# Optimization experiments

Measured on AMD Instinct MI355X. Metric: run time of the kernel, lower is better.

Reference implementation:

```python
import jax, jax.numpy as jnp
import numpy as np

N_NODES = 100000
N_EDGES = 1600000
IN_FEATS = 128
NUM_HEADS = 4
OUT_FEATS = 32
NUM_ETYPES = 8
DROP_BLOCKS = 4


def setup_inputs() -> dict:
    key = jax.random.key(0)
    k1, k2, k3, k4, k5 = jax.random.split(key, 5)
    feat = jax.random.normal(k1, (N_NODES, IN_FEATS), dtype=jnp.float32)
    e_feat = jax.random.randint(k2, (N_EDGES,), 0, NUM_ETYPES, dtype=jnp.int32)
    src = jax.random.randint(k3, (N_EDGES,), 0, N_NODES, dtype=jnp.int32)
    dst = jax.random.randint(k4, (N_EDGES,), 0, N_NODES, dtype=jnp.int32)
    kf, ke = jax.random.split(k5)
    # xavier_normal with relu gain for fc: std = gain * sqrt(2/(fan_in+fan_out))
    gain = float(np.sqrt(2.0))
    std = gain * float(np.sqrt(2.0 / (IN_FEATS + NUM_HEADS * OUT_FEATS)))
    fc_weight = jax.random.normal(kf, (NUM_HEADS * OUT_FEATS, IN_FEATS), dtype=jnp.float32) * std
    # edge_emb initialized with normal_()
    edge_emb = jax.random.normal(ke, (NUM_ETYPES, NUM_HEADS), dtype=jnp.float32)
    return {"feat": feat, "fc_weight": fc_weight, "edge_emb": edge_emb,
            "e_feat": e_feat, "src": src, "dst": dst, "drop_blocks": DROP_BLOCKS}


def _edge_softmax(e, dst, n_nodes):
    # segmented softmax over incoming edges per destination node, per head
    # e: (E, H)
    m = jax.ops.segment_max(e, dst, num_segments=n_nodes)      # (N, H)
    z = jnp.exp(e - m[dst])                                    # (E, H)
    s = jax.ops.segment_sum(z, dst, num_segments=n_nodes)      # (N, H)
    return z / s[dst]


def reference(feat, fc_weight, edge_emb, e_feat, src, dst, drop_blocks):
    n = feat.shape[0]
    H = edge_emb.shape[1]
    D = fc_weight.shape[0] // H
    # fc projection -> (N, H, D); feat_drop is identity (p=0 / eval)
    ft = (feat @ fc_weight.T).reshape(n, H, D)
    # edge type embedding logits (E, H)
    ee = edge_emb[e_feat]
    attn = _edge_softmax(ee, dst, n)                           # (E, H)
    # mcdropedge with attn_drop p=0: attn broadcast over blocks is identity scaling
    # u_mul_e + sum: gather src features, scale by attn, scatter-sum into dst
    msg = ft[src] * attn[:, :, None]                           # (E, H, D)
    rst = jax.ops.segment_sum(msg, dst, num_segments=n)        # (N, H, D)
    # attn returned with mcdropedge expansion shape (E, H, drop_blocks, 1)
    attn_out = jnp.broadcast_to(attn[:, :, None], (attn.shape[0], H, drop_blocks))[..., None]
    return rst, attn_out
```

## Files before the change

kernel.cpp:

```cpp
#include <hip/hip_runtime.h>


typedef short short8 __attribute__((ext_vector_type(8)));
typedef unsigned short ushort8 __attribute__((ext_vector_type(8)));
typedef float f32x4 __attribute__((ext_vector_type(4)));

__device__ inline unsigned short f2bf(float x) {
    unsigned u = __builtin_bit_cast(unsigned, x);
    u += 0x7FFFu + ((u >> 16) & 1u);
    return (unsigned short)(u >> 16);
}

__device__ inline void nt_store4(float* p, float a, float b, float c, float d) {
    f32x4 v = (f32x4){a, b, c, d};
    __builtin_nontemporal_store(v, (f32x4*)p);
}

__global__ __launch_bounds__(256) void k_bcnt(const int* __restrict__ dst,
                                              unsigned* __restrict__ gpart, int E) {
    __shared__ unsigned l[256];
    int tid = threadIdx.x;
    l[tid] = 0;
    __syncthreads();
    int base = blockIdx.x * 4096;
#pragma unroll
    for (int j = 0; j < 16; ++j) {
        int e = base + j * 256 + tid;
        if (e < E) atomicAdd(&l[(unsigned)dst[e] >> 9], 1u);
    }
    __syncthreads();
    gpart[blockIdx.x * 256 + tid] = l[tid];
}

__global__ __launch_bounds__(256) void k_bscan(const unsigned* __restrict__ gpart,
                                               int nchunk,
                                               unsigned* __restrict__ gbase,
                                               unsigned* __restrict__ gcur) {
    __shared__ unsigned s[256];
    int t = threadIdx.x;
    unsigned sum = 0;
    int r = 0;
    for (; r + 4 <= nchunk; r += 4) {
        unsigned a0 = gpart[(r + 0) * 256 + t];
        unsigned a1 = gpart[(r + 1) * 256 + t];
        unsigned a2 = gpart[(r + 2) * 256 + t];
        unsigned a3 = gpart[(r + 3) * 256 + t];
        sum += a0 + a1 + a2 + a3;
    }
    for (; r < nchunk; ++r) sum += gpart[r * 256 + t];
    unsigned orig = sum;
    s[t] = sum;
    __syncthreads();
    for (int of = 1; of < 256; of <<= 1) {
        unsigned v = (t >= of) ? s[t - of] : 0u;
        __syncthreads();
        s[t] += v;
        __syncthreads();
    }
    unsigned eb = s[t] - orig;
    gbase[t] = eb;
    gcur[t] = eb;
}

__global__ __launch_bounds__(256) void k_part(const int* __restrict__ src,
                                              const int* __restrict__ dst,
                                              const int* __restrict__ ef,
                                              unsigned* __restrict__ gcur,
                                              unsigned* __restrict__ csr2,
                                              int E, int nbuk) {
    __shared__ unsigned lcnt[256];
    __shared__ unsigned lbase[256];
    __shared__ unsigned lcur[256];
    __shared__ unsigned gw2[256];
    __shared__ unsigned stp[4096];
    __shared__ unsigned short stb[4096];
    int tid = threadIdx.x;
    lcnt[tid] = 0;
    __syncthreads();

    int cb = blockIdx.x * 4096;
    int cc = E - cb; if (cc > 4096) cc = 4096;

    unsigned pay[16];
    unsigned short bk[16];
#pragma unroll
    for (int j = 0; j < 16; ++j) {
        int idx = j * 256 + tid;
        if (idx < cc) {
            int e = cb + idx;
            unsigned d = (unsigned)dst[e];
            pay[j] = (unsigned)src[e] | ((unsigned)ef[e] << 17) | ((d & 511u) << 20);
            bk[j] = (unsigned short)(d >> 9);
            atomicAdd(&lcnt[bk[j]], 1u);
        }
    }
    __syncthreads();
    lbase[tid] = lcnt[tid];
    __syncthreads();
    for (int of = 1; of < 256; of <<= 1) {
        unsigned v = (tid >= of) ? lbase[tid - of] : 0u;
        __syncthreads();
        lbase[tid] += v;
        __syncthreads();
    }
    unsigned eb = lbase[tid] - lcnt[tid];
    __syncthreads();
    lbase[tid] = eb;
    lcur[tid] = eb;
    __syncthreads();
#pragma unroll
    for (int j = 0; j < 16; ++j) {
        int idx = j * 256 + tid;
        if (idx < cc) {
            unsigned lpos = atomicAdd(&lcur[bk[j]], 1u);
            stp[lpos] = pay[j];
            stb[lpos] = bk[j];
        }
    }
    if (tid < nbuk && lcnt[tid]) gw2[tid] = atomicAdd(&gcur[tid], lcnt[tid]);
    __syncthreads();
#pragma unroll
    for (int j = 0; j < 16; ++j) {
        int i = j * 256 + tid;
        if (i < cc) {
            unsigned b = stb[i];
            csr2[gw2[b] + (i - lbase[b])] = stp[i];
        }
    }
}

__global__ __launch_bounds__(256) void k_bsort2(const unsigned* __restrict__ csr2,
                                                const unsigned* __restrict__ gbase,
                                                const unsigned* __restrict__ gend,
                                                const float* __restrict__ emb,
                                                unsigned* __restrict__ csr,
                                                unsigned* __restrict__ offs,
                                                unsigned* __restrict__ deg,
                                                float* __restrict__ stats, int N) {
    __shared__ unsigned cnt8[512 * 8];
    __shared__ unsigned degL[512];
    __shared__ unsigned offsL[512];
    __shared__ unsigned curL[512];
    __shared__ unsigned tmp[256];
    __shared__ float se[32];
    int b = blockIdx.x, tid = threadIdx.x;
    if (tid < 32) se[tid] = emb[tid];
#pragma unroll
    for (int i = 0; i < 16; ++i) cnt8[i * 256 + tid] = 0u;
    __syncthreads();
    unsigned r0 = gbase[b], r1 = gend[b];
    for (unsigned i = r0 + tid; i < r1; i += 256) {
        unsigned en = csr2[i];
        atomicAdd(&cnt8[((en >> 20) & 511u) * 8u + ((en >> 17) & 7u)], 1u);
    }
    __syncthreads();
    int n0 = tid * 2, n1 = tid * 2 + 1;
    unsigned d0 = 0, d1 = 0;
#pragma unroll
    for (int k = 0; k < 8; ++k) { d0 += cnt8[n0 * 8 + k]; d1 += cnt8[n1 * 8 + k]; }
    degL[n0] = d0; degL[n1] = d1;
    tmp[tid] = d0 + d1;
    __syncthreads();
    for (int of = 1; of < 256; of <<= 1) {
        unsigned v = (tid >= of) ? tmp[tid - of] : 0u;
        __syncthreads();
        tmp[tid] += v;
        __syncthreads();
    }
    unsigned eb = tmp[tid] - (d0 + d1);
    offsL[n0] = eb;        curL[n0] = eb;
    offsL[n1] = eb + d0;   curL[n1] = eb + d0;
#pragma unroll
    for (int q = 0; q < 2; ++q) {
        int nl = tid * 2 + q;
        int gn = b * 512 + nl;
        if (gn < N) {
            offs[gn] = r0 + offsL[nl];
            unsigned dg = degL[nl];
            deg[gn] = dg;
            const unsigned* c = &cnt8[nl * 8];
#pragma unroll
            for (int h = 0; h < 4; ++h) {
                float m = -3.4e38f;
#pragma unroll
                for (int tt = 0; tt < 8; ++tt)
                    if (c[tt]) m = fmaxf(m, se[tt * 4 + h]);
                float s = 0.f;
#pragma unroll
                for (int tt = 0; tt < 8; ++tt)
                    if (c[tt]) s += (float)c[tt] * expf(se[tt * 4 + h] - m);
                stats[(size_t)gn * 8 + h] = m;
                stats[(size_t)gn * 8 + 4 + h] = dg ? (1.0f / s) : 0.0f;
            }
        }
    }
    __syncthreads();
    for (unsigned i = r0 + tid; i < r1; i += 256) {
        unsigned en = csr2[i];
        unsigned nlo = (en >> 20) & 511u;
        unsigned tt = (en >> 17) & 7u;
        unsigned pos = r0 + atomicAdd(&curL[nlo], 1u);
        csr[pos] = (en & 0x1FFFFu) | (tt << 20);
    }
}

__global__ __launch_bounds__(256) void k_attn_out(const int* __restrict__ e_feat,
                                                  const int* __restrict__ dst,
                                                  const float* __restrict__ emb,
                                                  const float* __restrict__ stats,
                                                  float* __restrict__ ao, int E) {
    __shared__ float av[4 * 257];
    int tid = threadIdx.x;
    int e = blockIdx.x * 256 + tid;
    float a0 = 0.f, a1 = 0.f, a2 = 0.f, a3 = 0.f;
    if (e < E) {
        int tt = e_feat[e];
        int d = dst[e];
        const float4* st4 = (const float4*)(stats + (size_t)d * 8);
        float4 m4 = st4[0], i4 = st4[1];
        float4 ee = *(const float4*)(emb + tt * 4);
        a0 = expf(ee.x - m4.x) * i4.x;
        a1 = expf(ee.y - m4.y) * i4.y;
        a2 = expf(ee.z - m4.z) * i4.z;
        a3 = expf(ee.w - m4.w) * i4.w;
    }
    av[0 * 257 + tid] = a0;
    av[1 * 257 + tid] = a1;
    av[2 * 257 + tid] = a2;
    av[3 * 257 + tid] = a3;
    __syncthreads();
    size_t base = (size_t)blockIdx.x * 1024;
    size_t lim = (size_t)E * 4;
#pragma unroll
    for (int r = 0; r < 4; ++r) {
        size_t g = base + r * 256 + tid;
        if (g < lim) {
            int gl = r * 256 + tid;
            float v = av[(gl & 3) * 257 + (gl >> 2)];
            nt_store4(ao + g * 4, v, v, v, v);
        }
    }
}

__global__ __launch_bounds__(256) void k_gemm_mfma(const float* __restrict__ feat,
                                                   const float* __restrict__ W,
                                                   unsigned short* __restrict__ ftb, int N) {
    __shared__ unsigned short Sb[128 * 136];
    int tid = threadIdx.x;
    int row0 = blockIdx.x * 128;

#pragma unroll
    for (int it = 0; it < 16; ++it) {
        int i = it * 1024 + tid * 4;
        int r = i >> 7, c = i & 127;
        unsigned swz = (unsigned)((r & 7) << 4);
        float4 w4 = *(const float4*)(W + i);
        ushort4 wb;
        wb.x = f2bf(w4.x); wb.y = f2bf(w4.y); wb.z = f2bf(w4.z); wb.w = f2bf(w4.w);
        *(ushort4*)((char*)Sb + (((unsigned)(r * 256 + c * 2)) ^ swz)) = wb;
    }
    __syncthreads();

    int wv = tid >> 6, lane = tid & 63;
    int rl = lane & 15;
    unsigned swz = (unsigned)((lane & 7) << 4);
    int kq = (lane >> 4) * 16;
    int ko = (lane >> 4) * 8;

    int ra0 = row0 + wv * 32 + rl;
    int ra1 = ra0 + 16;
    bool v0 = ra0 < N, v1 = ra1 < N;
    const float* ap0 = feat + (size_t)ra0 * 128 + ko;
    const float* ap1 = feat + (size_t)ra1 * 128 + ko;

    f32x4 acc[2][8];
#pragma unroll
    for (int rt = 0; rt < 2; ++rt)
#pragma unroll
        for (int jt = 0; jt < 8; ++jt)
            acc[rt][jt] = (f32x4){0.f, 0.f, 0.f, 0.f};

    const char* Bb = (const char*)Sb;
#pragma unroll
    for (int kk = 0; kk < 4; ++kk) {
        int kb = kk * 64 + kq;
        short8 a[2], bfr[8];
#pragma unroll
        for (int rt = 0; rt < 2; ++rt) {
            const float* ap = rt ? ap1 : ap0;
            bool v = rt ? v1 : v0;
            float4 lo = make_float4(0.f, 0.f, 0.f, 0.f), hi = lo;
            if (v) { lo = *(const float4*)(ap + kk * 32); hi = *(const float4*)(ap + kk * 32 + 4); }
            short8 t;
            t[0] = (short)f2bf(lo.x); t[1] = (short)f2bf(lo.y);
            t[2] = (short)f2bf(lo.z); t[3] = (short)f2bf(lo.w);
            t[4] = (short)f2bf(hi.x); t[5] = (short)f2bf(hi.y);
            t[6] = (short)f2bf(hi.z); t[7] = (short)f2bf(hi.w);
            a[rt] = t;
        }
#pragma unroll
        for (int jt = 0; jt < 8; ++jt)
            bfr[jt] = *(const short8*)(Bb + (((unsigned)((jt * 16 + rl) * 256 + kb)) ^ swz));
#pragma unroll
        for (int rt = 0; rt < 2; ++rt)
#pragma unroll
            for (int jt = 0; jt < 8; ++jt)
                acc[rt][jt] = __builtin_amdgcn_mfma_f32_16x16x32_bf16(a[rt], bfr[jt], acc[rt][jt], 0, 0, 0);
    }

    __syncthreads();
#pragma unroll
    for (int rt = 0; rt < 2; ++rt) {
        int rbase = wv * 32 + rt * 16 + ((lane >> 4) << 2);
#pragma unroll
        for (int jt = 0; jt < 8; ++jt) {
            int col = jt * 16 + rl;
#pragma unroll
            for (int rg = 0; rg < 4; ++rg)
                Sb[(rbase + rg) * 136 + col] = f2bf(acc[rt][jt][rg]);
        }
    }
    __syncthreads();
#pragma unroll
    for (int g = 0; g < 8; ++g) {
        int rloc = g * 16 + (tid >> 4);
        int cc = (tid & 15) * 8;
        int gr = row0 + rloc;
        if (gr < N) {
            ushort8 v = *(const ushort8*)(&Sb[rloc * 136 + cc]);
            *(ushort8*)(ftb + (size_t)gr * 128 + cc) = v;
        }
    }
}

__global__ __launch_bounds__(256) void k_agg(const unsigned* __restrict__ csr,
                                             const unsigned* __restrict__ offs,
                                             const unsigned* __restrict__ deg,
                                             const float* __restrict__ stats,
                                             const float* __restrict__ emb,
                                             const uint4* __restrict__ ft4,
                                             float* __restrict__ rst, int N) {
    __shared__ float wl[4 * 32];
    int tid = threadIdx.x;
    int wv = tid >> 6, lane = tid & 63;
    int n = blockIdx.x * 4 + wv;
    n = __builtin_amdgcn_readfirstlane(n);
    if (n < N && lane < 32) {
        int tt = lane >> 2, hh = lane & 3;
        float m = stats[(size_t)n * 8 + hh];
        float is = stats[(size_t)n * 8 + 4 + hh];
        wl[wv * 32 + lane] = expf(emb[tt * 4 + hh] - m) * is;
    }
    __syncthreads();
    if (n >= N) return;
    unsigned o = offs[n], dg = deg[n];
    int cl = lane & 15;
    int es = lane >> 4;
    int h = cl >> 2;
    const float* wlh = wl + wv * 32 + h;
    float acc[8];
#pragma unroll
    for (int i = 0; i < 8; ++i) acc[i] = 0.f;

    for (unsigned kb = 0; kb < dg; kb += 64) {
        unsigned rem = dg - kb; if (rem > 64) rem = 64;
        unsigned centry = 0;
        if (lane < (int)rem) centry = csr[o + kb + lane];
        unsigned g = 0;
        for (; g + 16 <= rem; g += 16) {
            uint4 f[4]; float a[4];
#pragma unroll
            for (int q = 0; q < 4; ++q) {
                unsigned e = __shfl(centry, (int)(g + q * 4 + es), 64);
                f[q] = ft4[(size_t)(e & 0xFFFFFu) * 16 + cl];
                a[q] = wlh[(e >> 20) * 4];
            }
#pragma unroll
            for (int q = 0; q < 4; ++q) {
                acc[0] = fmaf(a[q], __builtin_bit_cast(float, f[q].x << 16), acc[0]);
                acc[1] = fmaf(a[q], __builtin_bit_cast(float, f[q].x & 0xFFFF0000u), acc[1]);
                acc[2] = fmaf(a[q], __builtin_bit_cast(float, f[q].y << 16), acc[2]);
                acc[3] = fmaf(a[q], __builtin_bit_cast(float, f[q].y & 0xFFFF0000u), acc[3]);
                acc[4] = fmaf(a[q], __builtin_bit_cast(float, f[q].z << 16), acc[4]);
                acc[5] = fmaf(a[q], __builtin_bit_cast(float, f[q].z & 0xFFFF0000u), acc[5]);
                acc[6] = fmaf(a[q], __builtin_bit_cast(float, f[q].w << 16), acc[6]);
                acc[7] = fmaf(a[q], __builtin_bit_cast(float, f[q].w & 0xFFFF0000u), acc[7]);
            }
        }
        for (; g < rem; g += 4) {
            int eidx = (int)g + es;
            bool valid = eidx < (int)rem;
            unsigned e = __shfl(centry, valid ? eidx : (int)g, 64);
            uint4 f = ft4[(size_t)(e & 0xFFFFFu) * 16 + cl];
            float a = valid ? wlh[(e >> 20) * 4] : 0.f;
            acc[0] = fmaf(a, __builtin_bit_cast(float, f.x << 16), acc[0]);
            acc[1] = fmaf(a, __builtin_bit_cast(float, f.x & 0xFFFF0000u), acc[1]);
            acc[2] = fmaf(a, __builtin_bit_cast(float, f.y << 16), acc[2]);
            acc[3] = fmaf(a, __builtin_bit_cast(float, f.y & 0xFFFF0000u), acc[3]);
            acc[4] = fmaf(a, __builtin_bit_cast(float, f.z << 16), acc[4]);
            acc[5] = fmaf(a, __builtin_bit_cast(float, f.z & 0xFFFF0000u), acc[5]);
            acc[6] = fmaf(a, __builtin_bit_cast(float, f.w << 16), acc[6]);
            acc[7] = fmaf(a, __builtin_bit_cast(float, f.w & 0xFFFF0000u), acc[7]);
        }
    }
#pragma unroll
    for (int i = 0; i < 8; ++i) {
        acc[i] += __shfl_xor(acc[i], 16, 64);
        acc[i] += __shfl_xor(acc[i], 32, 64);
    }
    if (lane < 16) {
        float* op = rst + (size_t)n * 128 + cl * 8;
        nt_store4(op, acc[0], acc[1], acc[2], acc[3]);
        nt_store4(op + 4, acc[4], acc[5], acc[6], acc[7]);
    }
}

extern "C" void kernel_launch(void* const* d_in, const int* in_sizes, int n_in,
                              void* d_out, int out_size, void* d_ws, size_t ws_size,
                              hipStream_t stream) {
    const float* feat = (const float*)d_in[0];
    const float* W = (const float*)d_in[1];
    const float* emb = (const float*)d_in[2];
    const int* e_feat = (const int*)d_in[3];
    const int* src = (const int*)d_in[4];
    const int* dst = (const int*)d_in[5];
    int N = in_sizes[0] / 128;
    int E = in_sizes[3];
    int nbuk = (N + 511) >> 9;
    int nchunk = (E + 4095) / 4096;

    char* ws = (char*)d_ws;
    size_t off = 0;
    auto alloc = [&](size_t bytes) {
        void* p = ws + off;
        off = (off + bytes + 255) & ~(size_t)255;
        return p;
    };
    unsigned short* ftb = (unsigned short*)alloc((size_t)N * 128 * 2);
    float* stats = (float*)alloc((size_t)N * 8 * 4);
    unsigned* deg = (unsigned*)alloc((size_t)N * 4);
    unsigned* offs = (unsigned*)alloc((size_t)N * 4);
    unsigned* csr = (unsigned*)alloc((size_t)E * 4);
    unsigned* csr2 = (unsigned*)alloc((size_t)E * 4);
    unsigned* gpart = (unsigned*)alloc((size_t)nchunk * 256 * 4);
    unsigned* gbase = (unsigned*)alloc(256 * 4);
    unsigned* gcur = (unsigned*)alloc(256 * 4);

    float* rst = (float*)d_out;
    float* ao = (float*)d_out + (size_t)N * 128;

    k_bcnt<<<nchunk, 256, 0, stream>>>(dst, gpart, E);
    k_bscan<<<1, 256, 0, stream>>>(gpart, nchunk, gbase, gcur);
    k_part<<<nchunk, 256, 0, stream>>>(src, dst, e_feat, gcur, csr2, E, nbuk);
    k_bsort2<<<nbuk, 256, 0, stream>>>(csr2, gbase, gcur, emb, csr, offs, deg, stats, N);
    k_attn_out<<<(E + 255) / 256, 256, 0, stream>>>(e_feat, dst, emb, stats, ao, E);
    k_gemm_mfma<<<(N + 127) / 128, 256, 0, stream>>>(feat, W, ftb, N);
    k_agg<<<(N + 3) / 4, 256, 0, stream>>>(csr, offs, deg, stats, emb, (const uint4*)ftb, rst, N);
}
```

Before: 178.7 us.

## Merge partition with GEMM and aggregation with attn-out into shared launches

```diff
diff --git a/kernel.cpp b/kernel.cpp
--- a/kernel.cpp
+++ b/kernel.cpp
@@ -62,69 +62,160 @@
     gcur[t] = eb;
 }
 
-__global__ __launch_bounds__(256) void k_part(const int* __restrict__ src,
-                                              const int* __restrict__ dst,
-                                              const int* __restrict__ ef,
-                                              unsigned* __restrict__ gcur,
-                                              unsigned* __restrict__ csr2,
-                                              int E, int nbuk) {
-    __shared__ unsigned lcnt[256];
-    __shared__ unsigned lbase[256];
-    __shared__ unsigned lcur[256];
-    __shared__ unsigned gw2[256];
-    __shared__ unsigned stp[4096];
-    __shared__ unsigned short stb[4096];
+__global__ __launch_bounds__(256) void k_partgemm(
+        const int* __restrict__ src, const int* __restrict__ dst,
+        const int* __restrict__ ef, unsigned* __restrict__ gcur,
+        unsigned* __restrict__ csr2, int E, int nbuk, int partBlocks,
+        const float* __restrict__ feat, const float* __restrict__ W,
+        unsigned short* __restrict__ ftb, int N) {
+    __shared__ unsigned short Sb[128 * 136];
     int tid = threadIdx.x;
-    lcnt[tid] = 0;
-    __syncthreads();
-
-    int cb = blockIdx.x * 4096;
-    int cc = E - cb; if (cc > 4096) cc = 4096;
-
-    unsigned pay[16];
-    unsigned short bk[16];
-#pragma unroll
-    for (int j = 0; j < 16; ++j) {
-        int idx = j * 256 + tid;
-        if (idx < cc) {
-            int e = cb + idx;
-            unsigned d = (unsigned)dst[e];
-            pay[j] = (unsigned)src[e] | ((unsigned)ef[e] << 17) | ((d & 511u) << 20);
-            bk[j] = (unsigned short)(d >> 9);
-            atomicAdd(&lcnt[bk[j]], 1u);
-        }
-    }
-    __syncthreads();
-    lbase[tid] = lcnt[tid];
-    __syncthreads();
-    for (int of = 1; of < 256; of <<= 1) {
-        unsigned v = (tid >= of) ? lbase[tid - of] : 0u;
-        __syncthreads();
-        lbase[tid] += v;
-        __syncthreads();
-    }
-    unsigned eb = lbase[tid] - lcnt[tid];
-    __syncthreads();
-    lbase[tid] = eb;
-    lcur[tid] = eb;
-    __syncthreads();
-#pragma unroll
-    for (int j = 0; j < 16; ++j) {
-        int idx = j * 256 + tid;
-        if (idx < cc) {
-            unsigned lpos = atomicAdd(&lcur[bk[j]], 1u);
-            stp[lpos] = pay[j];
-            stb[lpos] = bk[j];
-        }
-    }
-    if (tid < nbuk && lcnt[tid]) gw2[tid] = atomicAdd(&gcur[tid], lcnt[tid]);
-    __syncthreads();
-#pragma unroll
-    for (int j = 0; j < 16; ++j) {
-        int i = j * 256 + tid;
-        if (i < cc) {
-            unsigned b = stb[i];
-            csr2[gw2[b] + (i - lbase[b])] = stp[i];
+
+    if (blockIdx.x < (unsigned)partBlocks) {
+        unsigned* lcnt = (unsigned*)Sb;
+        unsigned* lbase = lcnt + 256;
+        unsigned* lcur = lbase + 256;
+        unsigned* gw2 = lcur + 256;
+        unsigned* stp = gw2 + 256;
+        unsigned short* stb = (unsigned short*)(stp + 4096);
+        int bid = blockIdx.x;
+        lcnt[tid] = 0;
+        __syncthreads();
+
+        int cb = bid * 4096;
+        int cc = E - cb; if (cc > 4096) cc = 4096;
+
+        unsigned pay[16];
+        unsigned short bk[16];
+#pragma unroll
+        for (int j = 0; j < 16; ++j) {
+            int idx = j * 256 + tid;
+            if (idx < cc) {
+                int e = cb + idx;
+                unsigned d = (unsigned)dst[e];
+                pay[j] = (unsigned)src[e] | ((unsigned)ef[e] << 17) | ((d & 511u) << 20);
+                bk[j] = (unsigned short)(d >> 9);
+                atomicAdd(&lcnt[bk[j]], 1u);
+            }
+        }
+        __syncthreads();
+        lbase[tid] = lcnt[tid];
+        __syncthreads();
+        for (int of = 1; of < 256; of <<= 1) {
+            unsigned v = (tid >= of) ? lbase[tid - of] : 0u;
+            __syncthreads();
+            lbase[tid] += v;
+            __syncthreads();
+        }
+        unsigned eb = lbase[tid] - lcnt[tid];
+        __syncthreads();
+        lbase[tid] = eb;
+        lcur[tid] = eb;
+        __syncthreads();
+#pragma unroll
+        for (int j = 0; j < 16; ++j) {
+            int idx = j * 256 + tid;
+            if (idx < cc) {
+                unsigned lpos = atomicAdd(&lcur[bk[j]], 1u);
+                stp[lpos] = pay[j];
+                stb[lpos] = bk[j];
+            }
+        }
+        if (tid < nbuk && lcnt[tid]) gw2[tid] = atomicAdd(&gcur[tid], lcnt[tid]);
+        __syncthreads();
+#pragma unroll
+        for (int j = 0; j < 16; ++j) {
+            int i = j * 256 + tid;
+            if (i < cc) {
+                unsigned b = stb[i];
+                csr2[gw2[b] + (i - lbase[b])] = stp[i];
+            }
+        }
+        return;
+    }
+
+    int row0 = (blockIdx.x - partBlocks) * 128;
+
+#pragma unroll
+    for (int it = 0; it < 16; ++it) {
+        int i = it * 1024 + tid * 4;
+        int r = i >> 7, c = i & 127;
+        unsigned swz = (unsigned)((r & 7) << 4);
+        float4 w4 = *(const float4*)(W + i);
+        ushort4 wb;
+        wb.x = f2bf(w4.x); wb.y = f2bf(w4.y); wb.z = f2bf(w4.z); wb.w = f2bf(w4.w);
+        *(ushort4*)((char*)Sb + (((unsigned)(r * 256 + c * 2)) ^ swz)) = wb;
+    }
+    __syncthreads();
+
+    int wv = tid >> 6, lane = tid & 63;
+    int rl = lane & 15;
+    unsigned swz = (unsigned)((lane & 7) << 4);
+    int kq = (lane >> 4) * 16;
+    int ko = (lane >> 4) * 8;
+
+    int ra0 = row0 + wv * 32 + rl;
+    int ra1 = ra0 + 16;
+    bool v0 = ra0 < N, v1 = ra1 < N;
+    const float* ap0 = feat + (size_t)ra0 * 128 + ko;
+    const float* ap1 = feat + (size_t)ra1 * 128 + ko;
+
+    f32x4 acc[2][8];
+#pragma unroll
+    for (int rt = 0; rt < 2; ++rt)
+#pragma unroll
+        for (int jt = 0; jt < 8; ++jt)
+            acc[rt][jt] = (f32x4){0.f, 0.f, 0.f, 0.f};
+
+    const char* Bb = (const char*)Sb;
+#pragma unroll
+    for (int kk = 0; kk < 4; ++kk) {
+        int kb = kk * 64 + kq;
+        short8 a[2], bfr[8];
+#pragma unroll
+        for (int rt = 0; rt < 2; ++rt) {
+            const float* ap = rt ? ap1 : ap0;
+            bool v = rt ? v1 : v0;
+            float4 lo = make_float4(0.f, 0.f, 0.f, 0.f), hi = lo;
+            if (v) { lo = *(const float4*)(ap + kk * 32); hi = *(const float4*)(ap + kk * 32 + 4); }
+            short8 t;
+            t[0] = (short)f2bf(lo.x); t[1] = (short)f2bf(lo.y);
+            t[2] = (short)f2bf(lo.z); t[3] = (short)f2bf(lo.w);
+            t[4] = (short)f2bf(hi.x); t[5] = (short)f2bf(hi.y);
+            t[6] = (short)f2bf(hi.z); t[7] = (short)f2bf(hi.w);
+            a[rt] = t;
+        }
+#pragma unroll
+        for (int jt = 0; jt < 8; ++jt)
+            bfr[jt] = *(const short8*)(Bb + (((unsigned)((jt * 16 + rl) * 256 + kb)) ^ swz));
+#pragma unroll
+        for (int rt = 0; rt < 2; ++rt)
+#pragma unroll
+            for (int jt = 0; jt < 8; ++jt)
+                acc[rt][jt] = __builtin_amdgcn_mfma_f32_16x16x32_bf16(a[rt], bfr[jt], acc[rt][jt], 0, 0, 0);
+    }
+
+    __syncthreads();
+#pragma unroll
+    for (int rt = 0; rt < 2; ++rt) {
+        int rbase = wv * 32 + rt * 16 + ((lane >> 4) << 2);
+#pragma unroll
+        for (int jt = 0; jt < 8; ++jt) {
+            int col = jt * 16 + rl;
+#pragma unroll
+            for (int rg = 0; rg < 4; ++rg)
+                Sb[(rbase + rg) * 136 + col] = f2bf(acc[rt][jt][rg]);
+        }
+    }
+    __syncthreads();
+#pragma unroll
+    for (int g = 0; g < 8; ++g) {
+        int rloc = g * 16 + (tid >> 4);
+        int cc = (tid & 15) * 8;
+        int gr = row0 + rloc;
+        if (gr < N) {
+            ushort8 v = *(const ushort8*)(&Sb[rloc * 136 + cc]);
+            *(ushort8*)(ftb + (size_t)gr * 128 + cc) = v;
         }
     }
 }
@@ -204,144 +295,51 @@
     }
 }
 
-__global__ __launch_bounds__(256) void k_attn_out(const int* __restrict__ e_feat,
-                                                  const int* __restrict__ dst,
-                                                  const float* __restrict__ emb,
-                                                  const float* __restrict__ stats,
-                                                  float* __restrict__ ao, int E) {
-    __shared__ float av[4 * 257];
+__global__ __launch_bounds__(256) void k_aggattn(
+        const unsigned* __restrict__ csr, const unsigned* __restrict__ offs,
+        const unsigned* __restrict__ deg, const float* __restrict__ stats,
+        const float* __restrict__ emb, const uint4* __restrict__ ft4,
+        float* __restrict__ rst, int N, int aggBlocks,
+        const int* __restrict__ e_feat, const int* __restrict__ dst,
+        float* __restrict__ ao, int E) {
+    __shared__ float sbuf[4 * 257];
     int tid = threadIdx.x;
-    int e = blockIdx.x * 256 + tid;
-    float a0 = 0.f, a1 = 0.f, a2 = 0.f, a3 = 0.f;
-    if (e < E) {
-        int tt = e_feat[e];
-        int d = dst[e];
-        const float4* st4 = (const float4*)(stats + (size_t)d * 8);
-        float4 m4 = st4[0], i4 = st4[1];
-        float4 ee = *(const float4*)(emb + tt * 4);
-        a0 = expf(ee.x - m4.x) * i4.x;
-        a1 = expf(ee.y - m4.y) * i4.y;
-        a2 = expf(ee.z - m4.z) * i4.z;
-        a3 = expf(ee.w - m4.w) * i4.w;
-    }
-    av[0 * 257 + tid] = a0;
-    av[1 * 257 + tid] = a1;
-    av[2 * 257 + tid] = a2;
-    av[3 * 257 + tid] = a3;
-    __syncthreads();
-    size_t base = (size_t)blockIdx.x * 1024;
-    size_t lim = (size_t)E * 4;
-#pragma unroll
-    for (int r = 0; r < 4; ++r) {
-        size_t g = base + r * 256 + tid;
-        if (g < lim) {
-            int gl = r * 256 + tid;
-            float v = av[(gl & 3) * 257 + (gl >> 2)];
-            nt_store4(ao + g * 4, v, v, v, v);
-        }
-    }
-}
-
-__global__ __launch_bounds__(256) void k_gemm_mfma(const float* __restrict__ feat,
-                                                   const float* __restrict__ W,
-                                                   unsigned short* __restrict__ ftb, int N) {
-    __shared__ unsigned short Sb[128 * 136];
-    int tid = threadIdx.x;
-    int row0 = blockIdx.x * 128;
-
-#pragma unroll
-    for (int it = 0; it < 16; ++it) {
-        int i = it * 1024 + tid * 4;
-        int r = i >> 7, c = i & 127;
-        unsigned swz = (unsigned)((r & 7) << 4);
-        float4 w4 = *(const float4*)(W + i);
-        ushort4 wb;
-        wb.x = f2bf(w4.x); wb.y = f2bf(w4.y); wb.z = f2bf(w4.z); wb.w = f2bf(w4.w);
-        *(ushort4*)((char*)Sb + (((unsigned)(r * 256 + c * 2)) ^ swz)) = wb;
-    }
-    __syncthreads();
-
-    int wv = tid >> 6, lane = tid & 63;
-    int rl = lane & 15;
-    unsigned swz = (unsigned)((lane & 7) << 4);
-    int kq = (lane >> 4) * 16;
-    int ko = (lane >> 4) * 8;
-
-    int ra0 = row0 + wv * 32 + rl;
-    int ra1 = ra0 + 16;
-    bool v0 = ra0 < N, v1 = ra1 < N;
-    const float* ap0 = feat + (size_t)ra0 * 128 + ko;
-    const float* ap1 = feat + (size_t)ra1 * 128 + ko;
-
-    f32x4 acc[2][8];
-#pragma unroll
-    for (int rt = 0; rt < 2; ++rt)
-#pragma unroll
-        for (int jt = 0; jt < 8; ++jt)
-            acc[rt][jt] = (f32x4){0.f, 0.f, 0.f, 0.f};
-
-    const char* Bb = (const char*)Sb;
-#pragma unroll
-    for (int kk = 0; kk < 4; ++kk) {
-        int kb = kk * 64 + kq;
-        short8 a[2], bfr[8];
-#pragma unroll
-        for (int rt = 0; rt < 2; ++rt) {
-            const float* ap = rt ? ap1 : ap0;
-            bool v = rt ? v1 : v0;
-            float4 lo = make_float4(0.f, 0.f, 0.f, 0.f), hi = lo;
-            if (v) { lo = *(const float4*)(ap + kk * 32); hi = *(const float4*)(ap + kk * 32 + 4); }
-            short8 t;
-            t[0] = (short)f2bf(lo.x); t[1] = (short)f2bf(lo.y);
-            t[2] = (short)f2bf(lo.z); t[3] = (short)f2bf(lo.w);
-            t[4] = (short)f2bf(hi.x); t[5] = (short)f2bf(hi.y);
-            t[6] = (short)f2bf(hi.z); t[7] = (short)f2bf(hi.w);
-            a[rt] = t;
-        }
-#pragma unroll
-        for (int jt = 0; jt < 8; ++jt)
-            bfr[jt] = *(const short8*)(Bb + (((unsigned)((jt * 16 + rl) * 256 + kb)) ^ swz));
-#pragma unroll
-        for (int rt = 0; rt < 2; ++rt)
-#pragma unroll
-            for (int jt = 0; jt < 8; ++jt)
-                acc[rt][jt] = __builtin_amdgcn_mfma_f32_16x16x32_bf16(a[rt], bfr[jt], acc[rt][jt], 0, 0, 0);
-    }
-
-    __syncthreads();
-#pragma unroll
-    for (int rt = 0; rt < 2; ++rt) {
-        int rbase = wv * 32 + rt * 16 + ((lane >> 4) << 2);
-#pragma unroll
-        for (int jt = 0; jt < 8; ++jt) {
-            int col = jt * 16 + rl;
-#pragma unroll
-            for (int rg = 0; rg < 4; ++rg)
-                Sb[(rbase + rg) * 136 + col] = f2bf(acc[rt][jt][rg]);
-        }
-    }
-    __syncthreads();
-#pragma unroll
-    for (int g = 0; g < 8; ++g) {
-        int rloc = g * 16 + (tid >> 4);
-        int cc = (tid & 15) * 8;
-        int gr = row0 + rloc;
-        if (gr < N) {
-            ushort8 v = *(const ushort8*)(&Sb[rloc * 136 + cc]);
-            *(ushort8*)(ftb + (size_t)gr * 128 + cc) = v;
-        }
-    }
-}
-
-__global__ __launch_bounds__(256) void k_agg(const unsigned* __restrict__ csr,
-                                             const unsigned* __restrict__ offs,
-                                             const unsigned* __restrict__ deg,
-                                             const float* __restrict__ stats,
-                                             const float* __restrict__ emb,
-                                             const uint4* __restrict__ ft4,
-                                             float* __restrict__ rst, int N) {
-    __shared__ float wl[4 * 32];
-    int tid = threadIdx.x;
+
+    if (blockIdx.x >= (unsigned)aggBlocks) {
+        int bid = blockIdx.x - aggBlocks;
+        int e = bid * 256 + tid;
+        float a0 = 0.f, a1 = 0.f, a2 = 0.f, a3 = 0.f;
+        if (e < E) {
+            int tt = e_feat[e];
+            int d = dst[e];
+            const float4* st4 = (const float4*)(stats + (size_t)d * 8);
+            float4 m4 = st4[0], i4 = st4[1];
+            float4 ee = *(const float4*)(emb + tt * 4);
+            a0 = expf(ee.x - m4.x) * i4.x;
+            a1 = expf(ee.y - m4.y) * i4.y;
+            a2 = expf(ee.z - m4.z) * i4.z;
+            a3 = expf(ee.w - m4.w) * i4.w;
+        }
+        sbuf[0 * 257 + tid] = a0;
+        sbuf[1 * 257 + tid] = a1;
+        sbuf[2 * 257 + tid] = a2;
+        sbuf[3 * 257 + tid] = a3;
+        __syncthreads();
+        size_t base = (size_t)bid * 1024;
+        size_t lim = (size_t)E * 4;
+#pragma unroll
+        for (int r = 0; r < 4; ++r) {
+            size_t g = base + r * 256 + tid;
+            if (g < lim) {
+                int gl = r * 256 + tid;
+                float v = sbuf[(gl & 3) * 257 + (gl >> 2)];
+                nt_store4(ao + g * 4, v, v, v, v);
+            }
+        }
+        return;
+    }
+
+    float* wl = sbuf;
     int wv = tid >> 6, lane = tid & 63;
     int n = blockIdx.x * 4 + wv;
     n = __builtin_amdgcn_readfirstlane(n);
@@ -428,6 +426,9 @@
     int E = in_sizes[3];
     int nbuk = (N + 511) >> 9;
     int nchunk = (E + 4095) / 4096;
+    int gemmBlocks = (N + 127) / 128;
+    int aggBlocks = (N + 3) / 4;
+    int attnBlocks = (E + 255) / 256;
 
     char* ws = (char*)d_ws;
     size_t off = 0;
@@ -451,9 +452,10 @@
 
     k_bcnt<<<nchunk, 256, 0, stream>>>(dst, gpart, E);
     k_bscan<<<1, 256, 0, stream>>>(gpart, nchunk, gbase, gcur);
-    k_part<<<nchunk, 256, 0, stream>>>(src, dst, e_feat, gcur, csr2, E, nbuk);
+    k_partgemm<<<nchunk + gemmBlocks, 256, 0, stream>>>(
+        src, dst, e_feat, gcur, csr2, E, nbuk, nchunk, feat, W, ftb, N);
     k_bsort2<<<nbuk, 256, 0, stream>>>(csr2, gbase, gcur, emb, csr, offs, deg, stats, N);
-    k_attn_out<<<(E + 255) / 256, 256, 0, stream>>>(e_feat, dst, emb, stats, ao, E);
-    k_gemm_mfma<<<(N + 127) / 128, 256, 0, stream>>>(feat, W, ftb, N);
-    k_agg<<<(N + 3) / 4, 256, 0, stream>>>(csr, offs, deg, stats, emb, (const uint4*)ftb, rst, N);
-}
+    k_aggattn<<<aggBlocks + attnBlocks, 256, 0, stream>>>(
+        csr, offs, deg, stats, emb, (const uint4*)ftb, rst, N, aggBlocks,
+        e_feat, dst, ao, E);
+}
```

New measurement: 165.3 us. -7.5%, faster.
